# Kernel tuning notes

Hardware: AMD Instinct MI355X
Metric: run time of the kernel (lower is better)

Reference implementation:

```python
import jax, jax.numpy as jnp
import numpy as np
from jax.ops import segment_sum

N_GRAPHS, N_PER = 100, 1000
N = N_GRAPHS * N_PER
DEG = 32
E = N * DEG
RATIO = 0.8
K = int(np.ceil(RATIO * N_PER))  # 800, equal-size graphs -> fixed k
F_IN, F_MID, F_OUT = 128, 16, 256


def setup_inputs() -> dict:
    key = jax.random.key(0)
    ks = jax.random.split(key, 10)
    x = jax.random.normal(ks[0], (N, F_IN), dtype=jnp.float32)
    # intra-graph random edges
    epg = E // N_GRAPHS
    src_l = jax.random.randint(ks[1], (N_GRAPHS, epg), 0, N_PER)
    dst_l = jax.random.randint(ks[2], (N_GRAPHS, epg), 0, N_PER)
    offs = (jnp.arange(N_GRAPHS) * N_PER)[:, None]
    edge_index = jnp.stack([(src_l + offs).reshape(-1), (dst_l + offs).reshape(-1)]).astype(jnp.int32)
    batch = jnp.repeat(jnp.arange(N_GRAPHS, dtype=jnp.int32), N_PER)
    s = lambda fan: 1.0 / np.sqrt(fan)
    W1 = jax.random.normal(ks[3], (F_IN, F_MID), dtype=jnp.float32) * s(F_IN)
    b1 = jnp.zeros((F_MID,), dtype=jnp.float32)
    w_rel = jax.random.normal(ks[4], (F_MID, 1), dtype=jnp.float32) * s(F_MID)
    b_rel = jnp.zeros((1,), dtype=jnp.float32)
    w_root = jax.random.normal(ks[5], (F_MID, 1), dtype=jnp.float32) * s(F_MID)
    W2 = jax.random.normal(ks[6], (F_MID, F_OUT), dtype=jnp.float32) * s(F_MID)
    b2 = jnp.zeros((F_OUT,), dtype=jnp.float32)
    return {"x": x, "edge_index": edge_index, "batch": batch,
            "W1": W1, "b1": b1, "w_rel": w_rel, "b_rel": b_rel,
            "w_root": w_root, "W2": W2, "b2": b2}


def _gcn(x, src, dst, W, b, self_w, ew, n):
    # GCNConv with self-loops: D^{-1/2}(A+I)D^{-1/2} X W + b; masked variant
    deg = segment_sum(ew, dst, num_segments=n) + self_w
    dis = jnp.where(deg > 0, jax.lax.rsqrt(deg), 0.0)
    xw = x @ W
    coef = ew * dis[src] * dis[dst]                       # [E]
    agg = segment_sum(xw[src] * coef[:, None], dst, num_segments=n)
    agg = agg + xw * (self_w * dis * dis)[:, None]        # self-loop term
    return agg + b


def reference(x, edge_index, batch, W1, b1, w_rel, b_rel, w_root, W2, b2):
    src, dst = edge_index[0], edge_index[1]
    ones_n = jnp.ones((N,), dtype=x.dtype)
    ones_e = jnp.ones((src.shape[0],), dtype=x.dtype)
    # conv1 + relu
    h = jax.nn.relu(_gcn(x, src, dst, W1, b1, ones_n, ones_e, N))
    # SAGPooling score: GraphConv(16,1) -> tanh
    agg = segment_sum(h[src], dst, num_segments=N)
    score = jnp.tanh((agg @ w_rel + h @ w_root + b_rel)[:, 0])  # [N]
    # per-graph top-k (equal graph sizes -> fixed K), expressed as node mask
    sc2 = score.reshape(N_GRAPHS, N_PER)
    _, idx = jax.lax.top_k(sc2, K)
    mask = jnp.zeros((N_GRAPHS, N_PER), dtype=x.dtype)
    mask = mask.at[jnp.arange(N_GRAPHS)[:, None], idx].set(1.0).reshape(-1)  # [N]
    h = h * (score * mask)[:, None]                       # x[perm] * score[perm]
    em = mask[src] * mask[dst]                            # filter_adj as edge mask
    # conv2 + relu on surviving nodes only
    h2 = jax.nn.relu(_gcn(h, src, dst, W2, b2, mask, em, N)) * mask[:, None]
    # global mean pool over surviving nodes per graph
    sums = segment_sum(h2, batch, num_segments=N_GRAPHS)
    cnt = segment_sum(mask, batch, num_segments=N_GRAPHS)
    return sums / cnt[:, None]
```

## Files before the change

### kernel.cpp

```cpp
#include <hip/hip_runtime.h>
#include <math.h>

#define N_NODES 100000
#define NG 100
#define N_PER 1000
#define N_EDGES 3200000
#define EPG 32000
#define EPG4 8000
#define EPGP 35008
#define K_TOP 800
#define F_IN 128
#define F_MID 16
#define F_OUT 256
#define SENT 1000

typedef __attribute__((ext_vector_type(8))) short short8;
typedef __attribute__((ext_vector_type(4))) float floatx4;

__device__ __forceinline__ unsigned short f2bf(float x) {
    union { float f; unsigned int u; } c; c.f = x;
    unsigned int u = c.u;
    u = u + 0x7FFF + ((u >> 16) & 1);
    return (unsigned short)(u >> 16);
}
__device__ __forceinline__ void add4(float4& a, const float4 b) {
    a.x += b.x; a.y += b.y; a.z += b.z; a.w += b.w;
}
__device__ __forceinline__ int fidx4(int s, int l) {
    return s * 16 + ((4 * (l + ((s >> 1) & 3))) & 15);
}
__device__ __forceinline__ unsigned int fkey(float f) {
    unsigned int u = __float_as_uint(f);
    return (u & 0x80000000u) ? ~u : (u | 0x80000000u);
}

__global__ __launch_bounds__(1024) void k_front(const float* __restrict__ x,
    const float* __restrict__ W1, const int* __restrict__ ei,
    unsigned short* __restrict__ csr, int* __restrict__ cntG, int* __restrict__ rsG,
    float* __restrict__ dis1G, float* __restrict__ xw1)
{
    int b = blockIdx.x, t = threadIdx.x;
    if (b < NG) {
        __shared__ int cnts[N_PER];
        __shared__ int cur[N_PER];
        __shared__ int rs[N_PER];
        __shared__ int scan[1024];
        int g = b, ebase = g * EPG, nbase = g * N_PER;
        const int4* dst4 = (const int4*)(ei + N_EDGES + ebase);
        const int4* src4 = (const int4*)(ei + ebase);
        int4 dreg[8], sreg[8];
        int ni = 0;
        for (int i = t; i < EPG4; i += 1024) { dreg[ni] = dst4[i]; sreg[ni] = src4[i]; ni++; }
        if (t < N_PER) { cnts[t] = 0; cur[t] = 0; }
        __syncthreads();
        for (int i = 0; i < ni; i++) {
            atomicAdd(&cnts[dreg[i].x - nbase], 1);
            atomicAdd(&cnts[dreg[i].y - nbase], 1);
            atomicAdd(&cnts[dreg[i].z - nbase], 1);
            atomicAdd(&cnts[dreg[i].w - nbase], 1);
        }
        __syncthreads();
        int c = (t < N_PER) ? cnts[t] : 0;
        int c4 = (c + 3) & ~3;
        scan[t] = c4;
        __syncthreads();
        for (int dd = 1; dd < 1024; dd <<= 1) {
            int v = (t >= dd) ? scan[t - dd] : 0;
            __syncthreads();
            scan[t] += v;
            __syncthreads();
        }
        int exc = scan[t] - c4;
        unsigned short* cg = csr + (size_t)g * EPGP;
        if (t < N_PER) {
            rs[t] = exc; rsG[nbase + t] = exc; cntG[nbase + t] = c;
            dis1G[nbase + t] = rsqrtf((float)c + 1.0f);
            for (int q = c; q < c4; q++) cg[exc + q] = (unsigned short)SENT;
        }
        __syncthreads();
        for (int i = 0; i < ni; i++) {
            int dl, p;
            dl = dreg[i].x - nbase; p = rs[dl] + atomicAdd(&cur[dl], 1); cg[p] = (unsigned short)(sreg[i].x - nbase);
            dl = dreg[i].y - nbase; p = rs[dl] + atomicAdd(&cur[dl], 1); cg[p] = (unsigned short)(sreg[i].y - nbase);
            dl = dreg[i].z - nbase; p = rs[dl] + atomicAdd(&cur[dl], 1); cg[p] = (unsigned short)(sreg[i].z - nbase);
            dl = dreg[i].w - nbase; p = rs[dl] + atomicAdd(&cur[dl], 1); cg[p] = (unsigned short)(sreg[i].w - nbase);
        }
    } else {
        __shared__ float xs[64 * 132];
        __shared__ float wsm[F_IN * F_MID];
        long tile = b - NG;
        long n0 = tile * 64;
        int nmax = (int)((N_NODES - n0 < 64) ? (N_NODES - n0) : 64);
        const float* xp = x + n0 * F_IN;
        for (int i = t; i < nmax * F_IN; i += 1024) {
            int n = i >> 7, k = i & 127;
            xs[n * 132 + k] = xp[i];
        }
        for (int i = t; i < F_IN * F_MID; i += 1024) wsm[i] = W1[i];
        __syncthreads();
        int node = t >> 4, j = t & 15;
        if (node < nmax) {
            const float* xr = xs + node * 132;
            float acc = 0.f;
#pragma unroll 16
            for (int k = 0; k < F_IN; k++) acc += xr[k] * wsm[k * F_MID + j];
            xw1[(n0 + node) * F_MID + j] = acc;
        }
    }
}

__global__ __launch_bounds__(1024) void k_mega(const unsigned short* __restrict__ csr,
    const int* __restrict__ cntG, const int* __restrict__ rsG,
    const float* __restrict__ dis1G, const float* __restrict__ xw1,
    const float* __restrict__ b1, const float* __restrict__ w_rel,
    const float* __restrict__ b_rel, const float* __restrict__ w_root,
    const float* __restrict__ W2, const float* __restrict__ b2,
    float* __restrict__ out)
{
    __shared__ __align__(16) float feat[(N_PER + 1) * F_MID];
    __shared__ __align__(16) unsigned short fbf[N_PER * F_MID];
    __shared__ __align__(16) unsigned short w2t[F_OUT * F_MID];
    __shared__ float sc[N_PER];
    __shared__ float msk[N_PER + 1];
    __shared__ float wsrc[N_PER + 1];
    __shared__ float hw[N_PER + 1];
    __shared__ float hro[N_PER];
    __shared__ float dis2a[N_PER];
    __shared__ float dis1l[N_PER];
    __shared__ int cntl[N_PER];
    __shared__ int rsl[N_PER];
    __shared__ int hist[1024];
    __shared__ float partial[F_OUT];
    __shared__ int sh_b1, sh_r1, sh_b2, sh_r2, sh_len, sh_cntgt;
    __shared__ float sh_thr;

    int t = threadIdx.x, g = blockIdx.x;
    int nbase = g * N_PER;
    const unsigned short* cg = csr + (size_t)g * EPGP;
    int grp = t >> 2, l = t & 3;

    if (t < N_PER) { cntl[t] = cntG[nbase + t]; rsl[t] = rsG[nbase + t]; dis1l[t] = dis1G[nbase + t]; }
    if (t == 0) { sh_cntgt = 0; sh_len = 0; }
    for (int i = t; i < F_OUT * F_MID; i += 1024) {
        int f = i >> 4, jj = i & 15;
        w2t[i] = f2bf(W2[jj * F_OUT + f]);
    }
    __syncthreads();

    {
        const float4* xsrc = (const float4*)(xw1 + (size_t)nbase * F_MID);
        for (int i = t; i < N_PER * 4; i += 1024) {
            int n = i >> 2, q = i & 3;
            float4 v = xsrc[i];
            float d = dis1l[n];
            v.x *= d; v.y *= d; v.z *= d; v.w *= d;
            *(float4*)(feat + fidx4(n, q)) = v;
        }
        if (t < 4) { float4 z = {0.f, 0.f, 0.f, 0.f}; *(float4*)(feat + fidx4(SENT, t)) = z; }
    }
    __syncthreads();

    float4 b14 = *(const float4*)(b1 + 4 * l);
    float4 wr4 = *(const float4*)(w_rel + 4 * l);
    float4 wo4 = *(const float4*)(w_root + 4 * l);
    float brel = b_rel[0];

    float4 hreg[4];
#pragma unroll
    for (int rr = 0; rr < 4; rr++) {
        int n = grp + 256 * rr;
        if (n < N_PER) {
            int c4 = (cntl[n] + 3) & ~3;
            const unsigned short* cp = cg + rsl[n];
            float4 a0 = {0,0,0,0}, a1 = a0, a2 = a0, a3 = a0;
            for (int k = 0; k < c4; k += 4) {
                uint2 wv = *(const uint2*)(cp + k);
                int s0 = wv.x & 0xFFFF, s1 = wv.x >> 16, s2 = wv.y & 0xFFFF, s3 = wv.y >> 16;
                add4(a0, *(const float4*)(feat + fidx4(s0, l)));
                add4(a1, *(const float4*)(feat + fidx4(s1, l)));
                add4(a2, *(const float4*)(feat + fidx4(s2, l)));
                add4(a3, *(const float4*)(feat + fidx4(s3, l)));
            }
            add4(a0, a1); add4(a2, a3); add4(a0, a2);
            float4 sf = *(const float4*)(feat + fidx4(n, l));
            float di = dis1l[n];
            float4 hv;
            hv.x = fmaxf(fmaf(di, a0.x + sf.x, b14.x), 0.f);
            hv.y = fmaxf(fmaf(di, a0.y + sf.y, b14.y), 0.f);
            hv.z = fmaxf(fmaf(di, a0.z + sf.z, b14.z), 0.f);
            hv.w = fmaxf(fmaf(di, a0.w + sf.w, b14.w), 0.f);
            hreg[rr] = hv;
        }
    }
    __syncthreads();
#pragma unroll
    for (int rr = 0; rr < 4; rr++) {
        int n = grp + 256 * rr;
        if (n < N_PER) *(float4*)(feat + fidx4(n, l)) = hreg[rr];
    }
    __syncthreads();

#pragma unroll
    for (int rr = 0; rr < 4; rr++) {
        int n = grp + 256 * rr;
        if (n < N_PER) {
            float4 hv = *(const float4*)(feat + fidx4(n, l));
            float p1 = hv.x * wr4.x + hv.y * wr4.y + hv.z * wr4.z + hv.w * wr4.w;
            float p2 = hv.x * wo4.x + hv.y * wo4.y + hv.z * wo4.z + hv.w * wo4.w;
            p1 += __shfl_xor(p1, 1); p1 += __shfl_xor(p1, 2);
            p2 += __shfl_xor(p2, 1); p2 += __shfl_xor(p2, 2);
            if (l == 0) { hw[n] = p1; hro[n] = p2; }
        }
    }
    if (t == 0) hw[SENT] = 0.f;
    __syncthreads();

#pragma unroll
    for (int rr = 0; rr < 4; rr++) {
        int n = grp + 256 * rr;
        if (n < N_PER) {
            int c4 = (cntl[n] + 3) & ~3;
            const unsigned short* cp = cg + rsl[n];
            float sm = 0.f;
            for (int k = 0; k < c4; k += 4) {
                uint2 wv = *(const uint2*)(cp + k);
                int s = (l == 0) ? (int)(wv.x & 0xFFFF) : (l == 1) ? (int)(wv.x >> 16)
                      : (l == 2) ? (int)(wv.y & 0xFFFF) : (int)(wv.y >> 16);
                sm += hw[s];
            }
            sm += __shfl_xor(sm, 1); sm += __shfl_xor(sm, 2);
            if (l == 0) sc[n] = tanhf(sm + hro[n] + brel);
        }
    }
    __syncthreads();

    unsigned int mykey = (t < N_PER) ? fkey(sc[t]) : 0u;
    hist[t] = 0;
    __syncthreads();
    if (t < N_PER) atomicAdd(&hist[mykey >> 22], 1);
    __syncthreads();
    {
        int v0 = hist[t]; __syncthreads();
        hist[1023 - t] = v0; __syncthreads();
        for (int dd = 1; dd < 1024; dd <<= 1) {
            int v = (t >= dd) ? hist[t - dd] : 0;
            __syncthreads(); hist[t] += v; __syncthreads();
        }
        int Sb = hist[1023 - t];
        int Snext = (t == 1023) ? 0 : hist[1022 - t];
        if (Sb >= K_TOP && Snext < K_TOP) { sh_b1 = t; sh_r1 = K_TOP - Snext; }
    }
    __syncthreads();
    int b1v = sh_b1, r1 = sh_r1;
    hist[t] = 0;
    __syncthreads();
    if (t < N_PER && (int)(mykey >> 22) == b1v) atomicAdd(&hist[(mykey >> 12) & 1023], 1);
    __syncthreads();
    {
        int v0 = hist[t]; __syncthreads();
        hist[1023 - t] = v0; __syncthreads();
        for (int dd = 1; dd < 1024; dd <<= 1) {
            int v = (t >= dd) ? hist[t - dd] : 0;
            __syncthreads(); hist[t] += v; __syncthreads();
        }
        int Sb = hist[1023 - t];
        int Snext = (t == 1023) ? 0 : hist[1022 - t];
        if (Sb >= r1 && Snext < r1) { sh_b2 = t; sh_r2 = r1 - Snext; }
    }
    __syncthreads();
    unsigned int pref = ((unsigned int)b1v << 10) | (unsigned int)sh_b2;
    int r2 = sh_r2;
    __syncthreads();
    if (t < N_PER && (mykey >> 12) == pref) { int p = atomicAdd(&sh_len, 1); hist[p] = (int)mykey; }
    __syncthreads();
    {
        int L = sh_len;
        if (t < L) {
            unsigned int k0 = (unsigned int)hist[t];
            int gcnt = 0, ecnt = 0;
            for (int q2 = 0; q2 < L; q2++) {
                unsigned int kq = (unsigned int)hist[q2];
                gcnt += (kq > k0); ecnt += (kq == k0);
            }
            if (gcnt < r2 && r2 <= gcnt + ecnt)
                sh_thr = __uint_as_float((k0 & 0x80000000u) ? (k0 & 0x7FFFFFFFu) : ~k0);
        }
    }
    __syncthreads();
    float thr = sh_thr;

    {
        bool pred = (t < N_PER) && (sc[t] > thr);
        unsigned long long bal = __ballot(pred);
        if ((t & 63) == 0) atomicAdd(&sh_cntgt, (int)__popcll(bal));
    }
    __syncthreads();
    {
        int need = K_TOP - sh_cntgt;
        if (t < N_PER) {
            float v = sc[t];
            float mm;
            if (v > thr) mm = 1.f;
            else if (v < thr) mm = 0.f;
            else {
                int r = 0;
                for (int q2 = 0; q2 < t; q2++) if (sc[q2] == thr) r++;
                mm = (r < need) ? 1.f : 0.f;
            }
            msk[t] = mm;
        }
        if (t == 0) { msk[SENT] = 0.f; wsrc[SENT] = 0.f; }
    }
    __syncthreads();

#pragma unroll
    for (int rr = 0; rr < 4; rr++) {
        int n = grp + 256 * rr;
        if (n < N_PER) {
            int c4 = (cntl[n] + 3) & ~3;
            const unsigned short* cp = cg + rsl[n];
            float sm = 0.f;
            for (int k = 0; k < c4; k += 4) {
                uint2 wv = *(const uint2*)(cp + k);
                int s = (l == 0) ? (int)(wv.x & 0xFFFF) : (l == 1) ? (int)(wv.x >> 16)
                      : (l == 2) ? (int)(wv.y & 0xFFFF) : (int)(wv.y >> 16);
                sm += msk[s];
            }
            sm += __shfl_xor(sm, 1); sm += __shfl_xor(sm, 2);
            if (l == 0) {
                float d2 = msk[n] * (sm + 1.f);
                float di = (d2 > 0.f) ? rsqrtf(d2) : 0.f;
                dis2a[n] = di;
                wsrc[n] = sc[n] * msk[n] * di;
            }
        }
    }
    __syncthreads();

    for (int i = t; i < N_PER * 4; i += 1024) {
        int n = i >> 2, q = i & 3;
        float w = wsrc[n];
        float4* p = (float4*)(feat + fidx4(n, q));
        float4 v = *p;
        v.x *= w; v.y *= w; v.z *= w; v.w *= w;
        *p = v;
    }
    __syncthreads();

    float4 preg[4];
#pragma unroll
    for (int rr = 0; rr < 4; rr++) {
        int n = grp + 256 * rr;
        if (n < N_PER) {
            float di = dis2a[n];
            float4 pv = {0,0,0,0};
            if (di != 0.f) {
                int c4 = (cntl[n] + 3) & ~3;
                const unsigned short* cp = cg + rsl[n];
                float4 a0 = {0,0,0,0}, a1 = a0, a2 = a0, a3 = a0;
                for (int k = 0; k < c4; k += 4) {
                    uint2 wv = *(const uint2*)(cp + k);
                    int s0 = wv.x & 0xFFFF, s1 = wv.x >> 16, s2 = wv.y & 0xFFFF, s3 = wv.y >> 16;
                    add4(a0, *(const float4*)(feat + fidx4(s0, l)));
                    add4(a1, *(const float4*)(feat + fidx4(s1, l)));
                    add4(a2, *(const float4*)(feat + fidx4(s2, l)));
                    add4(a3, *(const float4*)(feat + fidx4(s3, l)));
                }
                add4(a0, a1); add4(a2, a3); add4(a0, a2);
                float4 sf = *(const float4*)(feat + fidx4(n, l));
                pv.x = di * (a0.x + sf.x);
                pv.y = di * (a0.y + sf.y);
                pv.z = di * (a0.z + sf.z);
                pv.w = di * (a0.w + sf.w);
            }
            preg[rr] = pv;
        }
    }
    __syncthreads();
#pragma unroll
    for (int rr = 0; rr < 4; rr++) {
        int n = grp + 256 * rr;
        if (n < N_PER) *(float4*)(feat + fidx4(n, l)) = preg[rr];
    }
    __syncthreads();

    for (int i = t; i < N_PER * 8; i += 1024) {
        int n = i >> 3, cp2 = (i & 7) * 2;
        int phys = n * 16 + ((cp2 + 4 * ((n >> 1) & 3)) & 15);
        float2 v = *(const float2*)(feat + phys);
        unsigned int pk = (unsigned int)f2bf(v.x) | ((unsigned int)f2bf(v.y) << 16);
        ((unsigned int*)fbf)[i] = pk;
    }
    __syncthreads();

    {
        int wave = t >> 6, lane = t & 63;
        int q = lane >> 4, fl = lane & 15;
        int half = wave >> 3, wcol = wave & 7;
        int c0 = 32 * wcol + fl, c1 = c0 + 16;
        float b2f0 = b2[c0], b2f1 = b2[c1];
        short8 bfrag0 = {0,0,0,0,0,0,0,0}, bfrag1 = bfrag0;
        if (q < 2) {
            bfrag0 = *(const short8*)(w2t + c0 * F_MID + q * 8);
            bfrag1 = *(const short8*)(w2t + c1 * F_MID + q * 8);
        }
        floatx4 zero = {0.f, 0.f, 0.f, 0.f};
        float acc0 = 0.f, acc1 = 0.f;
        int t0 = half ? 32 : 0, t1 = half ? 63 : 32;
        for (int tile = t0; tile < t1; tile++) {
            short8 afrag = {0,0,0,0,0,0,0,0};
            int na = tile * 16 + fl;
            if (q < 2 && na < N_PER)
                afrag = *(const short8*)(fbf + na * F_MID + q * 8);
            floatx4 d0 = __builtin_amdgcn_mfma_f32_16x16x32_bf16(afrag, bfrag0, zero, 0, 0, 0);
            floatx4 d1 = __builtin_amdgcn_mfma_f32_16x16x32_bf16(afrag, bfrag1, zero, 0, 0, 0);
#pragma unroll
            for (int r = 0; r < 4; r++) {
                int nd = tile * 16 + q * 4 + r;
                if (nd < N_PER) {
                    float m = msk[nd];
                    acc0 += m * fmaxf(d0[r] + b2f0, 0.f);
                    acc1 += m * fmaxf(d1[r] + b2f1, 0.f);
                }
            }
        }
        acc0 += __shfl_xor(acc0, 16); acc0 += __shfl_xor(acc0, 32);
        acc1 += __shfl_xor(acc1, 16); acc1 += __shfl_xor(acc1, 32);
        if (half == 0 && lane < 16) { partial[c0] = acc0; partial[c1] = acc1; }
        __syncthreads();
        if (half == 1 && lane < 16) {
            out[g * F_OUT + c0] = (partial[c0] + acc0) * (1.0f / (float)K_TOP);
            out[g * F_OUT + c1] = (partial[c1] + acc1) * (1.0f / (float)K_TOP);
        }
    }
}

extern "C" void kernel_launch(void* const* d_in, const int* in_sizes, int n_in,
                              void* d_out, int out_size, void* d_ws, size_t ws_size,
                              hipStream_t stream) {
    const float* x      = (const float*)d_in[0];
    const int*   ei     = (const int*)d_in[1];
    const float* W1     = (const float*)d_in[3];
    const float* b1     = (const float*)d_in[4];
    const float* w_rel  = (const float*)d_in[5];
    const float* b_rel  = (const float*)d_in[6];
    const float* w_root = (const float*)d_in[7];
    const float* W2     = (const float*)d_in[8];
    const float* b2     = (const float*)d_in[9];
    float* out = (float*)d_out;

    char* ws = (char*)d_ws;
    size_t o = 0;
    unsigned short* csr = (unsigned short*)(ws + o); o += (size_t)NG * EPGP * sizeof(unsigned short);
    int*   cntG  = (int*)(ws + o);   o += (size_t)N_NODES * sizeof(int);
    int*   rsG   = (int*)(ws + o);   o += (size_t)N_NODES * sizeof(int);
    float* dis1G = (float*)(ws + o); o += (size_t)N_NODES * sizeof(float);
    float* xw1   = (float*)(ws + o); o += (size_t)N_NODES * F_MID * sizeof(float);

    int gemm_blocks = (N_NODES + 63) / 64;
    k_front<<<NG + gemm_blocks, 1024, 0, stream>>>(x, W1, ei, csr, cntG, rsG, dis1G, xw1);
    k_mega<<<NG, 1024, 0, stream>>>(csr, cntG, rsG, dis1G, xw1,
                                    b1, w_rel, b_rel, w_root, W2, b2, out);
}
```

Baseline: 242.9 us.

## Split per-graph mega kernel into chunked conv1, mid, and conv2 kernels

Replaces the single 100-block per-graph mega kernel with three kernels. The two gather-heavy convolution stages run on 800 blocks, each covering a chunk of 128 nodes, and gather neighbour features from global memory instead of LDS. The top-k scoring stage keeps one block per graph. Intermediate h, scores, masks and normalisers are written to global workspace. The conv2 pooling now accumulates with atomicAdd into an output zeroed in k_mid. This aims to fix low GPU occupancy (100 blocks on a device with many more CUs), at the cost of extra launches, global round trips and atomics.

```diff
diff --git a/kernel.cpp b/kernel.cpp
--- a/kernel.cpp
+++ b/kernel.cpp
@@ -13,6 +13,8 @@
 #define F_MID 16
 #define F_OUT 256
 #define SENT 1000
+#define NCH 8
+#define CHN 128
 
 typedef __attribute__((ext_vector_type(8))) short short8;
 typedef __attribute__((ext_vector_type(4))) float floatx4;
@@ -26,9 +28,6 @@
 __device__ __forceinline__ void add4(float4& a, const float4 b) {
     a.x += b.x; a.y += b.y; a.z += b.z; a.w += b.w;
 }
-__device__ __forceinline__ int fidx4(int s, int l) {
-    return s * 16 + ((4 * (l + ((s >> 1) & 3))) & 15);
-}
 __device__ __forceinline__ unsigned int fkey(float f) {
     unsigned int u = __float_as_uint(f);
     return (u & 0x80000000u) ? ~u : (u | 0x80000000u);
@@ -36,7 +35,7 @@
 
 __global__ __launch_bounds__(1024) void k_front(const float* __restrict__ x,
     const float* __restrict__ W1, const int* __restrict__ ei,
-    unsigned short* __restrict__ csr, int* __restrict__ cntG, int* __restrict__ rsG,
+    unsigned short* __restrict__ csr, int* __restrict__ crG,
     float* __restrict__ dis1G, float* __restrict__ xw1)
 {
     int b = blockIdx.x, t = threadIdx.x;
@@ -46,6 +45,7 @@
         __shared__ int rs[N_PER];
         __shared__ int scan[1024];
         int g = b, ebase = g * EPG, nbase = g * N_PER;
+        if (b == 0 && t < F_MID) xw1[(size_t)N_NODES * F_MID + t] = 0.f;
         const int4* dst4 = (const int4*)(ei + N_EDGES + ebase);
         const int4* src4 = (const int4*)(ei + ebase);
         int4 dreg[8], sreg[8];
@@ -73,7 +73,8 @@
         int exc = scan[t] - c4;
         unsigned short* cg = csr + (size_t)g * EPGP;
         if (t < N_PER) {
-            rs[t] = exc; rsG[nbase + t] = exc; cntG[nbase + t] = c;
+            rs[t] = exc;
+            crG[nbase + t] = (c << 16) | exc;
             dis1G[nbase + t] = rsqrtf((float)c + 1.0f);
             for (int q = c; q < c4; q++) cg[exc + q] = (unsigned short)SENT;
         }
@@ -109,28 +110,76 @@
     }
 }
 
-__global__ __launch_bounds__(1024) void k_mega(const unsigned short* __restrict__ csr,
-    const int* __restrict__ cntG, const int* __restrict__ rsG,
+__global__ __launch_bounds__(512) void k_conv1(const unsigned short* __restrict__ csr,
+    const int* __restrict__ crG,
     const float* __restrict__ dis1G, const float* __restrict__ xw1,
     const float* __restrict__ b1, const float* __restrict__ w_rel,
-    const float* __restrict__ b_rel, const float* __restrict__ w_root,
-    const float* __restrict__ W2, const float* __restrict__ b2,
+    const float* __restrict__ w_root,
+    float* __restrict__ hG, float* __restrict__ hwG, float* __restrict__ hroG)
+{
+    __shared__ float dis1l[N_PER + 1];
+    int t = threadIdx.x, b = blockIdx.x;
+    int g = b % NG, chunk = b / NG;
+    int nbase = g * N_PER;
+    const unsigned short* cg = csr + (size_t)g * EPGP;
+    if (b == 0 && t < F_MID) hG[(size_t)N_NODES * F_MID + t] = 0.f;
+    for (int i = t; i < N_PER; i += 512) dis1l[i] = dis1G[nbase + i];
+    if (t == 0) dis1l[SENT] = 0.f;
+    __syncthreads();
+
+    int grp = t >> 2, l = t & 3;
+    int n = chunk * CHN + grp;
+    if (n >= N_PER) return;
+    int cr = crG[nbase + n];
+    int c4 = ((cr >> 16) + 3) & ~3;
+    const unsigned short* cp = cg + (cr & 0xFFFF);
+    float4 a0 = {0,0,0,0}, a1 = a0, a2 = a0, a3 = a0;
+    for (int k = 0; k < c4; k += 4) {
+        uint2 wv = *(const uint2*)(cp + k);
+        int s0 = wv.x & 0xFFFF, s1 = wv.x >> 16, s2 = wv.y & 0xFFFF, s3 = wv.y >> 16;
+        float4 v0 = *(const float4*)(xw1 + ((size_t)(nbase + s0) << 4) + 4 * l);
+        float4 v1 = *(const float4*)(xw1 + ((size_t)(nbase + s1) << 4) + 4 * l);
+        float4 v2 = *(const float4*)(xw1 + ((size_t)(nbase + s2) << 4) + 4 * l);
+        float4 v3 = *(const float4*)(xw1 + ((size_t)(nbase + s3) << 4) + 4 * l);
+        float w0 = dis1l[s0], w1 = dis1l[s1], w2 = dis1l[s2], w3 = dis1l[s3];
+        a0.x = fmaf(v0.x, w0, a0.x); a0.y = fmaf(v0.y, w0, a0.y); a0.z = fmaf(v0.z, w0, a0.z); a0.w = fmaf(v0.w, w0, a0.w);
+        a1.x = fmaf(v1.x, w1, a1.x); a1.y = fmaf(v1.y, w1, a1.y); a1.z = fmaf(v1.z, w1, a1.z); a1.w = fmaf(v1.w, w1, a1.w);
+        a2.x = fmaf(v2.x, w2, a2.x); a2.y = fmaf(v2.y, w2, a2.y); a2.z = fmaf(v2.z, w2, a2.z); a2.w = fmaf(v2.w, w2, a2.w);
+        a3.x = fmaf(v3.x, w3, a3.x); a3.y = fmaf(v3.y, w3, a3.y); a3.z = fmaf(v3.z, w3, a3.z); a3.w = fmaf(v3.w, w3, a3.w);
+    }
+    add4(a0, a1); add4(a2, a3); add4(a0, a2);
+    float dn = dis1l[n];
+    float4 sfr = *(const float4*)(xw1 + ((size_t)(nbase + n) << 4) + 4 * l);
+    float4 b14 = *(const float4*)(b1 + 4 * l);
+    float4 hv;
+    hv.x = fmaxf(fmaf(dn, fmaf(sfr.x, dn, a0.x), b14.x), 0.f);
+    hv.y = fmaxf(fmaf(dn, fmaf(sfr.y, dn, a0.y), b14.y), 0.f);
+    hv.z = fmaxf(fmaf(dn, fmaf(sfr.z, dn, a0.z), b14.z), 0.f);
+    hv.w = fmaxf(fmaf(dn, fmaf(sfr.w, dn, a0.w), b14.w), 0.f);
+    *(float4*)(hG + ((size_t)(nbase + n) << 4) + 4 * l) = hv;
+
+    float4 wr4 = *(const float4*)(w_rel + 4 * l);
+    float4 wo4 = *(const float4*)(w_root + 4 * l);
+    float p1 = hv.x * wr4.x + hv.y * wr4.y + hv.z * wr4.z + hv.w * wr4.w;
+    float p2 = hv.x * wo4.x + hv.y * wo4.y + hv.z * wo4.z + hv.w * wo4.w;
+    p1 += __shfl_xor(p1, 1); p1 += __shfl_xor(p1, 2);
+    p2 += __shfl_xor(p2, 1); p2 += __shfl_xor(p2, 2);
+    if (l == 0) { hwG[nbase + n] = p1; hroG[nbase + n] = p2; }
+}
+
+__global__ __launch_bounds__(1024) void k_mid(const unsigned short* __restrict__ csr,
+    const int* __restrict__ crG,
+    const float* __restrict__ hwG, const float* __restrict__ hroG,
+    const float* __restrict__ b_rel,
+    float* __restrict__ mskG, float* __restrict__ dis2G, float* __restrict__ wsrcG,
     float* __restrict__ out)
 {
-    __shared__ __align__(16) float feat[(N_PER + 1) * F_MID];
-    __shared__ __align__(16) unsigned short fbf[N_PER * F_MID];
-    __shared__ __align__(16) unsigned short w2t[F_OUT * F_MID];
+    __shared__ float hwl[N_PER + 1];
     __shared__ float sc[N_PER];
     __shared__ float msk[N_PER + 1];
-    __shared__ float wsrc[N_PER + 1];
-    __shared__ float hw[N_PER + 1];
-    __shared__ float hro[N_PER];
-    __shared__ float dis2a[N_PER];
-    __shared__ float dis1l[N_PER];
     __shared__ int cntl[N_PER];
     __shared__ int rsl[N_PER];
     __shared__ int hist[1024];
-    __shared__ float partial[F_OUT];
     __shared__ int sh_b1, sh_r1, sh_b2, sh_r2, sh_len, sh_cntgt;
     __shared__ float sh_thr;
 
@@ -139,80 +188,14 @@
     const unsigned short* cg = csr + (size_t)g * EPGP;
     int grp = t >> 2, l = t & 3;
 
-    if (t < N_PER) { cntl[t] = cntG[nbase + t]; rsl[t] = rsG[nbase + t]; dis1l[t] = dis1G[nbase + t]; }
-    if (t == 0) { sh_cntgt = 0; sh_len = 0; }
-    for (int i = t; i < F_OUT * F_MID; i += 1024) {
-        int f = i >> 4, jj = i & 15;
-        w2t[i] = f2bf(W2[jj * F_OUT + f]);
-    }
-    __syncthreads();
-
-    {
-        const float4* xsrc = (const float4*)(xw1 + (size_t)nbase * F_MID);
-        for (int i = t; i < N_PER * 4; i += 1024) {
-            int n = i >> 2, q = i & 3;
-            float4 v = xsrc[i];
-            float d = dis1l[n];
-            v.x *= d; v.y *= d; v.z *= d; v.w *= d;
-            *(float4*)(feat + fidx4(n, q)) = v;
-        }
-        if (t < 4) { float4 z = {0.f, 0.f, 0.f, 0.f}; *(float4*)(feat + fidx4(SENT, t)) = z; }
-    }
-    __syncthreads();
-
-    float4 b14 = *(const float4*)(b1 + 4 * l);
-    float4 wr4 = *(const float4*)(w_rel + 4 * l);
-    float4 wo4 = *(const float4*)(w_root + 4 * l);
+    if (t < N_PER) {
+        int cr = crG[nbase + t];
+        cntl[t] = cr >> 16; rsl[t] = cr & 0xFFFF;
+        hwl[t] = hwG[nbase + t];
+    }
+    if (t == 0) { sh_cntgt = 0; sh_len = 0; hwl[SENT] = 0.f; }
+    if (t < F_OUT) out[g * F_OUT + t] = 0.f;
     float brel = b_rel[0];
-
-    float4 hreg[4];
-#pragma unroll
-    for (int rr = 0; rr < 4; rr++) {
-        int n = grp + 256 * rr;
-        if (n < N_PER) {
-            int c4 = (cntl[n] + 3) & ~3;
-            const unsigned short* cp = cg + rsl[n];
-            float4 a0 = {0,0,0,0}, a1 = a0, a2 = a0, a3 = a0;
-            for (int k = 0; k < c4; k += 4) {
-                uint2 wv = *(const uint2*)(cp + k);
-                int s0 = wv.x & 0xFFFF, s1 = wv.x >> 16, s2 = wv.y & 0xFFFF, s3 = wv.y >> 16;
-                add4(a0, *(const float4*)(feat + fidx4(s0, l)));
-                add4(a1, *(const float4*)(feat + fidx4(s1, l)));
-                add4(a2, *(const float4*)(feat + fidx4(s2, l)));
-                add4(a3, *(const float4*)(feat + fidx4(s3, l)));
-            }
-            add4(a0, a1); add4(a2, a3); add4(a0, a2);
-            float4 sf = *(const float4*)(feat + fidx4(n, l));
-            float di = dis1l[n];
-            float4 hv;
-            hv.x = fmaxf(fmaf(di, a0.x + sf.x, b14.x), 0.f);
-            hv.y = fmaxf(fmaf(di, a0.y + sf.y, b14.y), 0.f);
-            hv.z = fmaxf(fmaf(di, a0.z + sf.z, b14.z), 0.f);
-            hv.w = fmaxf(fmaf(di, a0.w + sf.w, b14.w), 0.f);
-            hreg[rr] = hv;
-        }
-    }
-    __syncthreads();
-#pragma unroll
-    for (int rr = 0; rr < 4; rr++) {
-        int n = grp + 256 * rr;
-        if (n < N_PER) *(float4*)(feat + fidx4(n, l)) = hreg[rr];
-    }
-    __syncthreads();
-
-#pragma unroll
-    for (int rr = 0; rr < 4; rr++) {
-        int n = grp + 256 * rr;
-        if (n < N_PER) {
-            float4 hv = *(const float4*)(feat + fidx4(n, l));
-            float p1 = hv.x * wr4.x + hv.y * wr4.y + hv.z * wr4.z + hv.w * wr4.w;
-            float p2 = hv.x * wo4.x + hv.y * wo4.y + hv.z * wo4.z + hv.w * wo4.w;
-            p1 += __shfl_xor(p1, 1); p1 += __shfl_xor(p1, 2);
-            p2 += __shfl_xor(p2, 1); p2 += __shfl_xor(p2, 2);
-            if (l == 0) { hw[n] = p1; hro[n] = p2; }
-        }
-    }
-    if (t == 0) hw[SENT] = 0.f;
     __syncthreads();
 
 #pragma unroll
@@ -226,10 +209,10 @@
                 uint2 wv = *(const uint2*)(cp + k);
                 int s = (l == 0) ? (int)(wv.x & 0xFFFF) : (l == 1) ? (int)(wv.x >> 16)
                       : (l == 2) ? (int)(wv.y & 0xFFFF) : (int)(wv.y >> 16);
-                sm += hw[s];
+                sm += hwl[s];
             }
             sm += __shfl_xor(sm, 1); sm += __shfl_xor(sm, 2);
-            if (l == 0) sc[n] = tanhf(sm + hro[n] + brel);
+            if (l == 0) sc[n] = tanhf(sm + hroG[nbase + n] + brel);
         }
     }
     __syncthreads();
@@ -309,7 +292,7 @@
             }
             msk[t] = mm;
         }
-        if (t == 0) { msk[SENT] = 0.f; wsrc[SENT] = 0.f; }
+        if (t == 0) msk[SENT] = 0.f;
     }
     __syncthreads();
 
@@ -330,74 +313,85 @@
             if (l == 0) {
                 float d2 = msk[n] * (sm + 1.f);
                 float di = (d2 > 0.f) ? rsqrtf(d2) : 0.f;
-                dis2a[n] = di;
-                wsrc[n] = sc[n] * msk[n] * di;
-            }
-        }
-    }
-    __syncthreads();
-
-    for (int i = t; i < N_PER * 4; i += 1024) {
-        int n = i >> 2, q = i & 3;
-        float w = wsrc[n];
-        float4* p = (float4*)(feat + fidx4(n, q));
-        float4 v = *p;
-        v.x *= w; v.y *= w; v.z *= w; v.w *= w;
-        *p = v;
-    }
-    __syncthreads();
-
-    float4 preg[4];
-#pragma unroll
-    for (int rr = 0; rr < 4; rr++) {
-        int n = grp + 256 * rr;
-        if (n < N_PER) {
-            float di = dis2a[n];
-            float4 pv = {0,0,0,0};
-            if (di != 0.f) {
-                int c4 = (cntl[n] + 3) & ~3;
-                const unsigned short* cp = cg + rsl[n];
-                float4 a0 = {0,0,0,0}, a1 = a0, a2 = a0, a3 = a0;
-                for (int k = 0; k < c4; k += 4) {
-                    uint2 wv = *(const uint2*)(cp + k);
-                    int s0 = wv.x & 0xFFFF, s1 = wv.x >> 16, s2 = wv.y & 0xFFFF, s3 = wv.y >> 16;
-                    add4(a0, *(const float4*)(feat + fidx4(s0, l)));
-                    add4(a1, *(const float4*)(feat + fidx4(s1, l)));
-                    add4(a2, *(const float4*)(feat + fidx4(s2, l)));
-                    add4(a3, *(const float4*)(feat + fidx4(s3, l)));
-                }
-                add4(a0, a1); add4(a2, a3); add4(a0, a2);
-                float4 sf = *(const float4*)(feat + fidx4(n, l));
-                pv.x = di * (a0.x + sf.x);
-                pv.y = di * (a0.y + sf.y);
-                pv.z = di * (a0.z + sf.z);
-                pv.w = di * (a0.w + sf.w);
-            }
-            preg[rr] = pv;
-        }
-    }
-    __syncthreads();
-#pragma unroll
-    for (int rr = 0; rr < 4; rr++) {
-        int n = grp + 256 * rr;
-        if (n < N_PER) *(float4*)(feat + fidx4(n, l)) = preg[rr];
-    }
-    __syncthreads();
-
-    for (int i = t; i < N_PER * 8; i += 1024) {
-        int n = i >> 3, cp2 = (i & 7) * 2;
-        int phys = n * 16 + ((cp2 + 4 * ((n >> 1) & 3)) & 15);
-        float2 v = *(const float2*)(feat + phys);
-        unsigned int pk = (unsigned int)f2bf(v.x) | ((unsigned int)f2bf(v.y) << 16);
-        ((unsigned int*)fbf)[i] = pk;
+                mskG[nbase + n] = msk[n];
+                dis2G[nbase + n] = di;
+                wsrcG[nbase + n] = sc[n] * msk[n] * di;
+            }
+        }
+    }
+}
+
+__global__ __launch_bounds__(512) void k_conv2(const unsigned short* __restrict__ csr,
+    const int* __restrict__ crG,
+    const float* __restrict__ hG, const float* __restrict__ wsrcG,
+    const float* __restrict__ dis2G, const float* __restrict__ mskG,
+    const float* __restrict__ W2, const float* __restrict__ b2,
+    float* __restrict__ out)
+{
+    __shared__ float wsrcl[N_PER + 1];
+    __shared__ __align__(16) unsigned short fbf[CHN * F_MID];
+    __shared__ __align__(16) unsigned short w2t[F_OUT * F_MID];
+    __shared__ float mskl[CHN];
+    int t = threadIdx.x, b = blockIdx.x;
+    int g = b % NG, chunk = b / NG;
+    int nbase = g * N_PER, n0 = chunk * CHN;
+    const unsigned short* cg = csr + (size_t)g * EPGP;
+
+    for (int i = t; i < N_PER; i += 512) wsrcl[i] = wsrcG[nbase + i];
+    if (t == 0) wsrcl[SENT] = 0.f;
+    for (int i = t; i < F_OUT * F_MID; i += 512) {
+        int f = i >> 4, jj = i & 15;
+        w2t[i] = f2bf(W2[jj * F_OUT + f]);
+    }
+    __syncthreads();
+
+    int grp = t >> 2, l = t & 3;
+    int n = n0 + grp;
+    if (n < N_PER) {
+        float di = dis2G[nbase + n];
+        float4 pv = {0.f, 0.f, 0.f, 0.f};
+        if (di != 0.f) {
+            int cr = crG[nbase + n];
+            int c4 = ((cr >> 16) + 3) & ~3;
+            const unsigned short* cp = cg + (cr & 0xFFFF);
+            float4 a0 = {0,0,0,0}, a1 = a0, a2 = a0, a3 = a0;
+            for (int k = 0; k < c4; k += 4) {
+                uint2 wv = *(const uint2*)(cp + k);
+                int s0 = wv.x & 0xFFFF, s1 = wv.x >> 16, s2 = wv.y & 0xFFFF, s3 = wv.y >> 16;
+                float4 v0 = *(const float4*)(hG + ((size_t)(nbase + s0) << 4) + 4 * l);
+                float4 v1 = *(const float4*)(hG + ((size_t)(nbase + s1) << 4) + 4 * l);
+                float4 v2 = *(const float4*)(hG + ((size_t)(nbase + s2) << 4) + 4 * l);
+                float4 v3 = *(const float4*)(hG + ((size_t)(nbase + s3) << 4) + 4 * l);
+                float w0 = wsrcl[s0], w1 = wsrcl[s1], w2 = wsrcl[s2], w3 = wsrcl[s3];
+                a0.x = fmaf(v0.x, w0, a0.x); a0.y = fmaf(v0.y, w0, a0.y); a0.z = fmaf(v0.z, w0, a0.z); a0.w = fmaf(v0.w, w0, a0.w);
+                a1.x = fmaf(v1.x, w1, a1.x); a1.y = fmaf(v1.y, w1, a1.y); a1.z = fmaf(v1.z, w1, a1.z); a1.w = fmaf(v1.w, w1, a1.w);
+                a2.x = fmaf(v2.x, w2, a2.x); a2.y = fmaf(v2.y, w2, a2.y); a2.z = fmaf(v2.z, w2, a2.z); a2.w = fmaf(v2.w, w2, a2.w);
+                a3.x = fmaf(v3.x, w3, a3.x); a3.y = fmaf(v3.y, w3, a3.y); a3.z = fmaf(v3.z, w3, a3.z); a3.w = fmaf(v3.w, w3, a3.w);
+            }
+            add4(a0, a1); add4(a2, a3); add4(a0, a2);
+            float wn = wsrcl[n];
+            float4 hs = *(const float4*)(hG + ((size_t)(nbase + n) << 4) + 4 * l);
+            pv.x = di * fmaf(hs.x, wn, a0.x);
+            pv.y = di * fmaf(hs.y, wn, a0.y);
+            pv.z = di * fmaf(hs.z, wn, a0.z);
+            pv.w = di * fmaf(hs.w, wn, a0.w);
+        }
+        unsigned int pk0 = (unsigned int)f2bf(pv.x) | ((unsigned int)f2bf(pv.y) << 16);
+        unsigned int pk1 = (unsigned int)f2bf(pv.z) | ((unsigned int)f2bf(pv.w) << 16);
+        *(unsigned int*)(fbf + grp * F_MID + 4 * l) = pk0;
+        *(unsigned int*)(fbf + grp * F_MID + 4 * l + 2) = pk1;
+        if (l == 0) mskl[grp] = mskG[nbase + n];
+    } else {
+        *(unsigned int*)(fbf + grp * F_MID + 4 * l) = 0u;
+        *(unsigned int*)(fbf + grp * F_MID + 4 * l + 2) = 0u;
+        if (l == 0) mskl[grp] = 0.f;
     }
     __syncthreads();
 
     {
         int wave = t >> 6, lane = t & 63;
         int q = lane >> 4, fl = lane & 15;
-        int half = wave >> 3, wcol = wave & 7;
-        int c0 = 32 * wcol + fl, c1 = c0 + 16;
+        int c0 = 32 * wave + fl, c1 = c0 + 16;
         float b2f0 = b2[c0], b2f1 = b2[c1];
         short8 bfrag0 = {0,0,0,0,0,0,0,0}, bfrag1 = bfrag0;
         if (q < 2) {
@@ -406,31 +400,26 @@
         }
         floatx4 zero = {0.f, 0.f, 0.f, 0.f};
         float acc0 = 0.f, acc1 = 0.f;
-        int t0 = half ? 32 : 0, t1 = half ? 63 : 32;
-        for (int tile = t0; tile < t1; tile++) {
+        for (int tile = 0; tile < CHN / 16; tile++) {
             short8 afrag = {0,0,0,0,0,0,0,0};
             int na = tile * 16 + fl;
-            if (q < 2 && na < N_PER)
+            if (q < 2)
                 afrag = *(const short8*)(fbf + na * F_MID + q * 8);
             floatx4 d0 = __builtin_amdgcn_mfma_f32_16x16x32_bf16(afrag, bfrag0, zero, 0, 0, 0);
             floatx4 d1 = __builtin_amdgcn_mfma_f32_16x16x32_bf16(afrag, bfrag1, zero, 0, 0, 0);
 #pragma unroll
             for (int r = 0; r < 4; r++) {
                 int nd = tile * 16 + q * 4 + r;
-                if (nd < N_PER) {
-                    float m = msk[nd];
-                    acc0 += m * fmaxf(d0[r] + b2f0, 0.f);
-                    acc1 += m * fmaxf(d1[r] + b2f1, 0.f);
-                }
+                float m = mskl[nd];
+                acc0 += m * fmaxf(d0[r] + b2f0, 0.f);
+                acc1 += m * fmaxf(d1[r] + b2f1, 0.f);
             }
         }
         acc0 += __shfl_xor(acc0, 16); acc0 += __shfl_xor(acc0, 32);
         acc1 += __shfl_xor(acc1, 16); acc1 += __shfl_xor(acc1, 32);
-        if (half == 0 && lane < 16) { partial[c0] = acc0; partial[c1] = acc1; }
-        __syncthreads();
-        if (half == 1 && lane < 16) {
-            out[g * F_OUT + c0] = (partial[c0] + acc0) * (1.0f / (float)K_TOP);
-            out[g * F_OUT + c1] = (partial[c1] + acc1) * (1.0f / (float)K_TOP);
+        if (lane < 16) {
+            atomicAdd(&out[g * F_OUT + c0], acc0 * (1.0f / (float)K_TOP));
+            atomicAdd(&out[g * F_OUT + c1], acc1 * (1.0f / (float)K_TOP));
         }
     }
 }
@@ -451,14 +440,21 @@
 
     char* ws = (char*)d_ws;
     size_t o = 0;
-    unsigned short* csr = (unsigned short*)(ws + o); o += (size_t)NG * EPGP * sizeof(unsigned short);
-    int*   cntG  = (int*)(ws + o);   o += (size_t)N_NODES * sizeof(int);
-    int*   rsG   = (int*)(ws + o);   o += (size_t)N_NODES * sizeof(int);
-    float* dis1G = (float*)(ws + o); o += (size_t)N_NODES * sizeof(float);
-    float* xw1   = (float*)(ws + o); o += (size_t)N_NODES * F_MID * sizeof(float);
+    auto nxt = [&](size_t bytes) { void* p = ws + o; o += (bytes + 255) & ~(size_t)255; return p; };
+    unsigned short* csr = (unsigned short*)nxt((size_t)NG * EPGP * sizeof(unsigned short));
+    int*   crG   = (int*)nxt((size_t)N_NODES * sizeof(int));
+    float* dis1G = (float*)nxt((size_t)N_NODES * sizeof(float));
+    float* xw1   = (float*)nxt(((size_t)N_NODES + 1) * F_MID * sizeof(float));
+    float* hG    = (float*)nxt(((size_t)N_NODES + 1) * F_MID * sizeof(float));
+    float* hwG   = (float*)nxt((size_t)N_NODES * sizeof(float));
+    float* hroG  = (float*)nxt((size_t)N_NODES * sizeof(float));
+    float* mskG  = (float*)nxt((size_t)N_NODES * sizeof(float));
+    float* dis2G = (float*)nxt((size_t)N_NODES * sizeof(float));
+    float* wsrcG = (float*)nxt((size_t)N_NODES * sizeof(float));
 
     int gemm_blocks = (N_NODES + 63) / 64;
-    k_front<<<NG + gemm_blocks, 1024, 0, stream>>>(x, W1, ei, csr, cntG, rsG, dis1G, xw1);
-    k_mega<<<NG, 1024, 0, stream>>>(csr, cntG, rsG, dis1G, xw1,
-                                    b1, w_rel, b_rel, w_root, W2, b2, out);
-}
+    k_front<<<NG + gemm_blocks, 1024, 0, stream>>>(x, W1, ei, csr, crG, dis1G, xw1);
+    k_conv1<<<NG * NCH, 512, 0, stream>>>(csr, crG, dis1G, xw1, b1, w_rel, w_root, hG, hwG, hroG);
+    k_mid<<<NG, 1024, 0, stream>>>(csr, crG, hwG, hroG, b_rel, mskG, dis2G, wsrcG, out);
+    k_conv2<<<NG * NCH, 512, 0, stream>>>(csr, crG, hG, wsrcG, dis2G, mskG, W2, b2, out);
+}
```

New measurement: 252.1 us. 3.8% more time.
